# Kernel tuning notes

Hardware: AMD Instinct MI355X
Metric: run time of the kernel (lower is better)

## Reference

```python
import jax, jax.numpy as jnp
import numpy as np

N = 50000
E = 800000
IN_CH = 128
HID = 32
HEADS = 8
OUT_CH = 64
NEG_SLOPE = 0.2  # PyG GATConv default


def setup_inputs() -> dict:
    key = jax.random.key(0)
    ks = jax.random.split(key, 12)
    x = jax.random.normal(ks[0], (N, IN_CH), dtype=jnp.float32)
    edge_index = jax.random.randint(ks[1], (2, E), 0, N, dtype=jnp.int64)
    s = 0.1
    return {
        "x": x,
        "edge_index": edge_index,
        "W1": jax.random.normal(ks[2], (IN_CH, HEADS * HID), dtype=jnp.float32) * s,
        "att_src1": jax.random.normal(ks[3], (HEADS, HID), dtype=jnp.float32) * s,
        "att_dst1": jax.random.normal(ks[4], (HEADS, HID), dtype=jnp.float32) * s,
        "b1": jnp.zeros((HEADS * HID,), dtype=jnp.float32),
        "W2": jax.random.normal(ks[5], (HEADS * HID, OUT_CH), dtype=jnp.float32) * s,
        "att_src2": jax.random.normal(ks[6], (1, OUT_CH), dtype=jnp.float32) * s,
        "att_dst2": jax.random.normal(ks[7], (1, OUT_CH), dtype=jnp.float32) * s,
        "b2": jnp.zeros((OUT_CH,), dtype=jnp.float32),
    }


def _gat_layer(x, src, dst, n, W, a_src, a_dst, b, concat):
    # x: [N, F_in]; src/dst: [E']; W: [F_in, H*C]; a_*: [H, C]
    H, C = a_src.shape
    h = (x @ W).reshape(-1, H, C)                       # [N, H, C]
    alpha_s = jnp.einsum('nhc,hc->nh', h, a_src)        # [N, H]
    alpha_d = jnp.einsum('nhc,hc->nh', h, a_dst)        # [N, H]
    alpha = alpha_s[src] + alpha_d[dst]                 # [E', H]
    alpha = jax.nn.leaky_relu(alpha, NEG_SLOPE)
    # segment (per-destination-node) softmax over incoming edges
    m = jax.ops.segment_max(alpha, dst, num_segments=n)     # [n, H]
    e = jnp.exp(alpha - m[dst])
    denom = jax.ops.segment_sum(e, dst, num_segments=n)     # [n, H]
    coef = e / denom[dst]                                   # [E', H]
    msg = h[src] * coef[:, :, None]                         # [E', H, C]
    out = jax.ops.segment_sum(msg, dst, num_segments=n)     # [n, H, C]
    out = out.reshape(n, H * C) if concat else out.mean(axis=1)
    return out + b


def reference(x, edge_index, W1, att_src1, att_dst1, b1, W2, att_src2, att_dst2, b2):
    n = x.shape[0]
    # PyG GATConv default: add self-loops
    loop = jnp.arange(n, dtype=edge_index.dtype)
    src = jnp.concatenate([edge_index[0], loop])
    dst = jnp.concatenate([edge_index[1], loop])
    # eval mode: F.dropout and attention dropout are identity
    h = _gat_layer(x, src, dst, n, W1, att_src1, att_dst1, b1, concat=True)
    h = jax.nn.elu(h)
    out = _gat_layer(h, src, dst, n, W2, att_src2, att_dst2, b2, concat=False)
    return out
```

## Files before the change

### kernel.cpp

```cpp
#include <hip/hip_runtime.h>
#include <hip/hip_bf16.h>
#include <math.h>

#define N_NODES 50000
#define N_EDGES 800000
#define E_TOT   (N_EDGES + N_NODES)
#define IN_CH 128
#define HID 32
#define HEADS 8
#define OUT_CH 64
#define NEG_SLOPE 0.2f
#define NBLK 196
#define RBLK 3321
#define G1BLK 3125
#define G2BLK 782
#define ABLK 12500
#define LOG2E 1.4426950408889634f

typedef __attribute__((ext_vector_type(8))) short bf16x8;
typedef __attribute__((ext_vector_type(4))) float f32x4;

__device__ __forceinline__ float lrelu(float x) { return x > 0.f ? x : NEG_SLOPE * x; }
__device__ __forceinline__ float explrelu(float z) {
    return exp2f(fmaxf(z * LOG2E, z * (NEG_SLOPE * LOG2E)));
}

__device__ __forceinline__ unsigned short f2bf(float f) {
    unsigned int u = __float_as_uint(f);
    unsigned int r = (u + 0x7FFFu + ((u >> 16) & 1u)) >> 16;
    return (unsigned short)r;
}
__device__ __forceinline__ float bf2f(unsigned short u) {
    return __uint_as_float(((unsigned int)u) << 16);
}
__device__ __forceinline__ float bflo(unsigned int u) {
    return __uint_as_float(u << 16);
}
__device__ __forceinline__ float bfhi(unsigned int u) {
    return __uint_as_float(u & 0xFFFF0000u);
}

__global__ void w1cast_kernel(const float* __restrict__ W1,
                              unsigned short* __restrict__ W1t) {
    int i = blockIdx.x * 256 + threadIdx.x;
    int col = i >> 7, k = i & 127;
    W1t[i] = f2bf(W1[k * 256 + col]);
}

__device__ __forceinline__ void gemm1_body(
    int blk, int t,
    const float* __restrict__ x, const unsigned short* __restrict__ W1t,
    const float* __restrict__ att_s, const float* __restrict__ att_d,
    unsigned short* __restrict__ h1b, float* __restrict__ as1, float* __restrict__ ad1) {
    int lane = t & 63;
    int w = t >> 6;
    int lrow = lane & 15;
    int kg = lane >> 4;
    int row0 = blk * 16;
    int gr = row0 + lrow;
    f32x4 acc0 = {0.f, 0.f, 0.f, 0.f};
    f32x4 acc1 = {0.f, 0.f, 0.f, 0.f};
    f32x4 acc2 = {0.f, 0.f, 0.f, 0.f};
    f32x4 acc3 = {0.f, 0.f, 0.f, 0.f};
#pragma unroll
    for (int ks = 0; ks < 4; ++ks) {
        const float* ap = &x[(size_t)gr * IN_CH + ks * 32 + kg * 8];
        float4 a0 = *(const float4*)ap;
        float4 a1 = *(const float4*)(ap + 4);
        union { bf16x8 v; unsigned int u[4]; } A;
        A.u[0] = ((unsigned)f2bf(a0.y) << 16) | f2bf(a0.x);
        A.u[1] = ((unsigned)f2bf(a0.w) << 16) | f2bf(a0.z);
        A.u[2] = ((unsigned)f2bf(a1.y) << 16) | f2bf(a1.x);
        A.u[3] = ((unsigned)f2bf(a1.w) << 16) | f2bf(a1.z);
        union { bf16x8 v; uint4 u; } B0, B1, B2, B3;
        int kb = ks * 32 + kg * 8;
        B0.u = *(const uint4*)&W1t[(size_t)(w * 64 + 0 * 16 + lrow) * IN_CH + kb];
        B1.u = *(const uint4*)&W1t[(size_t)(w * 64 + 1 * 16 + lrow) * IN_CH + kb];
        B2.u = *(const uint4*)&W1t[(size_t)(w * 64 + 2 * 16 + lrow) * IN_CH + kb];
        B3.u = *(const uint4*)&W1t[(size_t)(w * 64 + 3 * 16 + lrow) * IN_CH + kb];
        acc0 = __builtin_amdgcn_mfma_f32_16x16x32_bf16(A.v, B0.v, acc0, 0, 0, 0);
        acc1 = __builtin_amdgcn_mfma_f32_16x16x32_bf16(A.v, B1.v, acc1, 0, 0, 0);
        acc2 = __builtin_amdgcn_mfma_f32_16x16x32_bf16(A.v, B2.v, acc2, 0, 0, 0);
        acc3 = __builtin_amdgcn_mfma_f32_16x16x32_bf16(A.v, B3.v, acc3, 0, 0, 0);
    }
    float s0 = att_s[w * 64 + 0 * 16 + lrow], d0 = att_d[w * 64 + 0 * 16 + lrow];
    float s1 = att_s[w * 64 + 1 * 16 + lrow], d1 = att_d[w * 64 + 1 * 16 + lrow];
    float s2 = att_s[w * 64 + 2 * 16 + lrow], d2 = att_d[w * 64 + 2 * 16 + lrow];
    float s3 = att_s[w * 64 + 3 * 16 + lrow], d3 = att_d[w * 64 + 3 * 16 + lrow];
#pragma unroll
    for (int r = 0; r < 4; ++r) {
        int orow = row0 + kg * 4 + r;
        h1b[(size_t)orow * 256 + w * 64 +  0 + lrow] = f2bf(acc0[r]);
        h1b[(size_t)orow * 256 + w * 64 + 16 + lrow] = f2bf(acc1[r]);
        h1b[(size_t)orow * 256 + w * 64 + 32 + lrow] = f2bf(acc2[r]);
        h1b[(size_t)orow * 256 + w * 64 + 48 + lrow] = f2bf(acc3[r]);
        float p0 = acc0[r] * s0 + acc1[r] * s1;
        float q0 = acc0[r] * d0 + acc1[r] * d1;
        float p1 = acc2[r] * s2 + acc3[r] * s3;
        float q1 = acc2[r] * d2 + acc3[r] * d3;
        p0 += __shfl_xor(p0, 1); q0 += __shfl_xor(q0, 1);
        p1 += __shfl_xor(p1, 1); q1 += __shfl_xor(q1, 1);
        p0 += __shfl_xor(p0, 2); q0 += __shfl_xor(q0, 2);
        p1 += __shfl_xor(p1, 2); q1 += __shfl_xor(q1, 2);
        p0 += __shfl_xor(p0, 4); q0 += __shfl_xor(q0, 4);
        p1 += __shfl_xor(p1, 4); q1 += __shfl_xor(q1, 4);
        p0 += __shfl_xor(p0, 8); q0 += __shfl_xor(q0, 8);
        p1 += __shfl_xor(p1, 8); q1 += __shfl_xor(q1, 8);
        if (lrow == 0) {
            as1[orow * HEADS + 2 * w]     = p0;
            ad1[orow * HEADS + 2 * w]     = q0;
            as1[orow * HEADS + 2 * w + 1] = p1;
            ad1[orow * HEADS + 2 * w + 1] = q1;
        }
    }
}

__global__ __launch_bounds__(256) void fused1_kernel(
    const int* __restrict__ ei, int* __restrict__ deg2, int* __restrict__ rank,
    const float* __restrict__ x, const unsigned short* __restrict__ W1t,
    const float* __restrict__ att_s, const float* __restrict__ att_d,
    unsigned short* __restrict__ h1b, float* __restrict__ as1, float* __restrict__ ad1,
    const float* __restrict__ W2, unsigned short* __restrict__ W2t) {
    int b = blockIdx.x;
    if (b < RBLK) {
        int e = b * 256 + threadIdx.x;
        if (e < E_TOT) {
            int d = (e < N_EDGES) ? ei[N_EDGES + e] : (e - N_EDGES);
            rank[e] = atomicAdd(&deg2[d * 16], 1);
        }
    } else if (b < RBLK + G1BLK) {
        gemm1_body(b - RBLK, threadIdx.x, x, W1t, att_s, att_d, h1b, as1, ad1);
    } else {
        int i = (b - RBLK - G1BLK) * 256 + threadIdx.x;
        int col = i >> 8, k = i & 255;
        W2t[i] = f2bf(W2[k * 64 + col]);
    }
}

__global__ void scan1_kernel(const int* __restrict__ deg2, int* __restrict__ off,
                             int* __restrict__ bsum) {
    __shared__ int s[256];
    int b = blockIdx.x, t = threadIdx.x, g = b * 256 + t;
    int v = (g < N_NODES) ? deg2[g * 16] : 0;
    s[t] = v;
    __syncthreads();
    for (int d = 1; d < 256; d <<= 1) {
        int o = (t >= d) ? s[t - d] : 0;
        __syncthreads();
        s[t] += o;
        __syncthreads();
    }
    if (g < N_NODES) off[g] = s[t] - v;
    if (t == 255) bsum[b] = s[t];
}

__global__ void scan2_kernel(int* __restrict__ bsum, int nb) {
    __shared__ int s[256];
    int t = threadIdx.x;
    int v = (t < nb) ? bsum[t] : 0;
    s[t] = v;
    __syncthreads();
    for (int d = 1; d < 256; d <<= 1) {
        int o = (t >= d) ? s[t - d] : 0;
        __syncthreads();
        s[t] += o;
        __syncthreads();
    }
    if (t < nb) bsum[t] = s[t] - v;
}

__global__ void scan3_kernel(int* __restrict__ off, const int* __restrict__ bsum) {
    int b = blockIdx.x, t = threadIdx.x, g = b * 256 + t;
    if (g < N_NODES) off[g] += bsum[b];
    if (g == 0) off[N_NODES] = E_TOT;
}

__global__ void place_kernel(const int* __restrict__ ei, const int* __restrict__ off,
                             const int* __restrict__ rank, int* __restrict__ ssrc) {
    int e = blockIdx.x * blockDim.x + threadIdx.x;
    if (e >= E_TOT) return;
    int s, d;
    if (e < N_EDGES) { s = ei[e]; d = ei[N_EDGES + e]; }
    else             { s = d = e - N_EDGES; }
    ssrc[off[d] + rank[e]] = s;
}

__global__ __launch_bounds__(256) void agg1_kernel(
    const int* __restrict__ off, const int* __restrict__ ssrc,
    const unsigned short* __restrict__ h1b, const float* __restrict__ as1,
    const float* __restrict__ ad1, const float* __restrict__ b1,
    unsigned short* __restrict__ houtb) {
    int t = threadIdx.x;
    int lane = t & 63;
    int n = blockIdx.x * 4 + (t >> 6);
    int h    = lane >> 3;
    int e8   = lane & 7;
    int c    = lane & 31;
    int hh   = c >> 2;
    int half = lane >> 5;
    int start = off[n], end = off[n + 1];
    int last = end - 1;
    float ad_w = ad1[n * HEADS + e8];
    float acc[8];
#pragma unroll
    for (int j = 0; j < 8; ++j) acc[j] = 0.f;
    float den = 0.f;
    int sv = ssrc[min(start + e8, last)];
    int se = __shfl(sv, h);
    float av = as1[se * HEADS + e8];
    const unsigned short* base = h1b + c * 8;
    uint4 g0 = *(const uint4*)&base[(unsigned)__shfl(sv, 0 + half) * 256];
    uint4 g1 = *(const uint4*)&base[(unsigned)__shfl(sv, 2 + half) * 256];
    uint4 g2 = *(const uint4*)&base[(unsigned)__shfl(sv, 4 + half) * 256];
    uint4 g3 = *(const uint4*)&base[(unsigned)__shfl(sv, 6 + half) * 256];
    for (int i = start; i < end; i += 8) {
        int inext = i + 8;
        int sv_n = ssrc[min(inext + e8, last)];
        int se_n = __shfl(sv_n, h);
        float av_n = as1[se_n * HEADS + e8];
        uint4 n0 = *(const uint4*)&base[(unsigned)__shfl(sv_n, 0 + half) * 256];
        uint4 n1 = *(const uint4*)&base[(unsigned)__shfl(sv_n, 2 + half) * 256];
        uint4 n2 = *(const uint4*)&base[(unsigned)__shfl(sv_n, 4 + half) * 256];
        uint4 n3 = *(const uint4*)&base[(unsigned)__shfl(sv_n, 6 + half) * 256];
        float wv = explrelu(av + ad_w);
        float w0 = __shfl(wv, (0 + half) * 8 + hh);
        float w1 = __shfl(wv, (2 + half) * 8 + hh);
        float w2 = __shfl(wv, (4 + half) * 8 + hh);
        float w3 = __shfl(wv, (6 + half) * 8 + hh);
        w0 = (i + 0 + half < end) ? w0 : 0.f;
        w1 = (i + 2 + half < end) ? w1 : 0.f;
        w2 = (i + 4 + half < end) ? w2 : 0.f;
        w3 = (i + 6 + half < end) ? w3 : 0.f;
        den += w0 + w1 + w2 + w3;
        acc[0] = fmaf(w0, bflo(g0.x), acc[0]); acc[1] = fmaf(w0, bfhi(g0.x), acc[1]);
        acc[2] = fmaf(w0, bflo(g0.y), acc[2]); acc[3] = fmaf(w0, bfhi(g0.y), acc[3]);
        acc[4] = fmaf(w0, bflo(g0.z), acc[4]); acc[5] = fmaf(w0, bfhi(g0.z), acc[5]);
        acc[6] = fmaf(w0, bflo(g0.w), acc[6]); acc[7] = fmaf(w0, bfhi(g0.w), acc[7]);
        acc[0] = fmaf(w1, bflo(g1.x), acc[0]); acc[1] = fmaf(w1, bfhi(g1.x), acc[1]);
        acc[2] = fmaf(w1, bflo(g1.y), acc[2]); acc[3] = fmaf(w1, bfhi(g1.y), acc[3]);
        acc[4] = fmaf(w1, bflo(g1.z), acc[4]); acc[5] = fmaf(w1, bfhi(g1.z), acc[5]);
        acc[6] = fmaf(w1, bflo(g1.w), acc[6]); acc[7] = fmaf(w1, bfhi(g1.w), acc[7]);
        acc[0] = fmaf(w2, bflo(g2.x), acc[0]); acc[1] = fmaf(w2, bfhi(g2.x), acc[1]);
        acc[2] = fmaf(w2, bflo(g2.y), acc[2]); acc[3] = fmaf(w2, bfhi(g2.y), acc[3]);
        acc[4] = fmaf(w2, bflo(g2.z), acc[4]); acc[5] = fmaf(w2, bfhi(g2.z), acc[5]);
        acc[6] = fmaf(w2, bflo(g2.w), acc[6]); acc[7] = fmaf(w2, bfhi(g2.w), acc[7]);
        acc[0] = fmaf(w3, bflo(g3.x), acc[0]); acc[1] = fmaf(w3, bfhi(g3.x), acc[1]);
        acc[2] = fmaf(w3, bflo(g3.y), acc[2]); acc[3] = fmaf(w3, bfhi(g3.y), acc[3]);
        acc[4] = fmaf(w3, bflo(g3.z), acc[4]); acc[5] = fmaf(w3, bfhi(g3.z), acc[5]);
        acc[6] = fmaf(w3, bflo(g3.w), acc[6]); acc[7] = fmaf(w3, bfhi(g3.w), acc[7]);
        g0 = n0; g1 = n1; g2 = n2; g3 = n3;
        sv = sv_n; av = av_n;
    }
#pragma unroll
    for (int j = 0; j < 8; ++j) acc[j] += __shfl_xor(acc[j], 32);
    den += __shfl_xor(den, 32);
    if (lane < 32) {
        float r = __builtin_amdgcn_rcpf(den);
        float4 b0 = *(const float4*)&b1[c * 8];
        float4 b4 = *(const float4*)&b1[c * 8 + 4];
        float v0 = fmaf(acc[0], r, b0.x);
        float v1 = fmaf(acc[1], r, b0.y);
        float v2 = fmaf(acc[2], r, b0.z);
        float v3 = fmaf(acc[3], r, b0.w);
        float v4 = fmaf(acc[4], r, b4.x);
        float v5 = fmaf(acc[5], r, b4.y);
        float v6 = fmaf(acc[6], r, b4.z);
        float v7 = fmaf(acc[7], r, b4.w);
        v0 = v0 > 0.f ? v0 : expm1f(v0);
        v1 = v1 > 0.f ? v1 : expm1f(v1);
        v2 = v2 > 0.f ? v2 : expm1f(v2);
        v3 = v3 > 0.f ? v3 : expm1f(v3);
        v4 = v4 > 0.f ? v4 : expm1f(v4);
        v5 = v5 > 0.f ? v5 : expm1f(v5);
        v6 = v6 > 0.f ? v6 : expm1f(v6);
        v7 = v7 > 0.f ? v7 : expm1f(v7);
        uint4 ob;
        ob.x = (unsigned)f2bf(v0) | ((unsigned)f2bf(v1) << 16);
        ob.y = (unsigned)f2bf(v2) | ((unsigned)f2bf(v3) << 16);
        ob.z = (unsigned)f2bf(v4) | ((unsigned)f2bf(v5) << 16);
        ob.w = (unsigned)f2bf(v6) | ((unsigned)f2bf(v7) << 16);
        *(uint4*)&houtb[(unsigned)n * 256 + c * 8] = ob;
    }
}

__global__ __launch_bounds__(256) void gemm2_mfma(
    const unsigned short* __restrict__ hinb, const unsigned short* __restrict__ W2t,
    const float* __restrict__ att_s2, const float* __restrict__ att_d2,
    unsigned short* __restrict__ h2b, float* __restrict__ as2, float* __restrict__ ad2) {
    int t = threadIdx.x;
    int lane = t & 63;
    int w = t >> 6;
    int lrow = lane & 15;
    int kg = lane >> 4;
    int row0 = blockIdx.x * 64 + w * 16;
    int gr = min(row0 + lrow, N_NODES - 1);
    f32x4 acc0 = {0.f, 0.f, 0.f, 0.f};
    f32x4 acc1 = {0.f, 0.f, 0.f, 0.f};
    f32x4 acc2 = {0.f, 0.f, 0.f, 0.f};
    f32x4 acc3 = {0.f, 0.f, 0.f, 0.f};
#pragma unroll
    for (int ks = 0; ks < 8; ++ks) {
        int kb = ks * 32 + kg * 8;
        union { bf16x8 v; uint4 u; } A, B0, B1, B2, B3;
        A.u  = *(const uint4*)&hinb[(size_t)gr * 256 + kb];
        B0.u = *(const uint4*)&W2t[(size_t)(0 * 16 + lrow) * 256 + kb];
        B1.u = *(const uint4*)&W2t[(size_t)(1 * 16 + lrow) * 256 + kb];
        B2.u = *(const uint4*)&W2t[(size_t)(2 * 16 + lrow) * 256 + kb];
        B3.u = *(const uint4*)&W2t[(size_t)(3 * 16 + lrow) * 256 + kb];
        acc0 = __builtin_amdgcn_mfma_f32_16x16x32_bf16(A.v, B0.v, acc0, 0, 0, 0);
        acc1 = __builtin_amdgcn_mfma_f32_16x16x32_bf16(A.v, B1.v, acc1, 0, 0, 0);
        acc2 = __builtin_amdgcn_mfma_f32_16x16x32_bf16(A.v, B2.v, acc2, 0, 0, 0);
        acc3 = __builtin_amdgcn_mfma_f32_16x16x32_bf16(A.v, B3.v, acc3, 0, 0, 0);
    }
    float s0 = att_s2[ 0 + lrow], d0 = att_d2[ 0 + lrow];
    float s1 = att_s2[16 + lrow], d1 = att_d2[16 + lrow];
    float s2 = att_s2[32 + lrow], d2 = att_d2[32 + lrow];
    float s3 = att_s2[48 + lrow], d3 = att_d2[48 + lrow];
#pragma unroll
    for (int r = 0; r < 4; ++r) {
        int orow = row0 + kg * 4 + r;
        float p = acc0[r] * s0 + acc1[r] * s1 + acc2[r] * s2 + acc3[r] * s3;
        float q = acc0[r] * d0 + acc1[r] * d1 + acc2[r] * d2 + acc3[r] * d3;
        p += __shfl_xor(p, 1); q += __shfl_xor(q, 1);
        p += __shfl_xor(p, 2); q += __shfl_xor(q, 2);
        p += __shfl_xor(p, 4); q += __shfl_xor(q, 4);
        p += __shfl_xor(p, 8); q += __shfl_xor(q, 8);
        if (orow < N_NODES) {
            h2b[(size_t)orow * 64 +  0 + lrow] = f2bf(acc0[r]);
            h2b[(size_t)orow * 64 + 16 + lrow] = f2bf(acc1[r]);
            h2b[(size_t)orow * 64 + 32 + lrow] = f2bf(acc2[r]);
            h2b[(size_t)orow * 64 + 48 + lrow] = f2bf(acc3[r]);
            if (lrow == 0) { as2[orow] = p; ad2[orow] = q; }
        }
    }
}

__global__ __launch_bounds__(256) void agg2_kernel(
    const int* __restrict__ off, const int* __restrict__ ssrc,
    const unsigned short* __restrict__ h2b, const float* __restrict__ as2,
    const float* __restrict__ ad2, const float* __restrict__ b2,
    float* __restrict__ out) {
    int t = threadIdx.x;
    int lane = t & 63;
    int e8 = lane & 7;
    int q = lane & 15;
    int quarter = lane >> 4;
    int n = blockIdx.x * 4 + (t >> 6);
    int start = off[n], end = off[n + 1];
    int last = end - 1;
    float adv = ad2[n];
    float acc[4];
#pragma unroll
    for (int j = 0; j < 4; ++j) acc[j] = 0.f;
    float den = 0.f;
    int sv = ssrc[min(start + e8, last)];
    float av = as2[sv];
    for (int i = start; i < end; i += 8) {
        int inext = i + 8;
        int sv_n = ssrc[min(inext + e8, last)];
        float av_n = as2[sv_n];
        float wv = explrelu(av + adv);
#pragma unroll
        for (int k = 0; k < 2; ++k) {
            int me = 4 * k + quarter;
            float wj = __shfl(wv, me);
            int   sj = __shfl(sv, me);
            wj = (i + me < end) ? wj : 0.f;
            uint2 u = *(const uint2*)&h2b[(unsigned)sj * 64 + q * 4];
            den += wj;
            acc[0] = fmaf(wj, bflo(u.x), acc[0]);
            acc[1] = fmaf(wj, bfhi(u.x), acc[1]);
            acc[2] = fmaf(wj, bflo(u.y), acc[2]);
            acc[3] = fmaf(wj, bfhi(u.y), acc[3]);
        }
        sv = sv_n; av = av_n;
    }
#pragma unroll
    for (int j = 0; j < 4; ++j) {
        acc[j] += __shfl_xor(acc[j], 16);
        acc[j] += __shfl_xor(acc[j], 32);
    }
    den += __shfl_xor(den, 16);
    den += __shfl_xor(den, 32);
    if (lane < 16) {
        float r = __builtin_amdgcn_rcpf(den);
        float4 bv = *(const float4*)&b2[q * 4];
        float4 o;
        o.x = fmaf(acc[0], r, bv.x);
        o.y = fmaf(acc[1], r, bv.y);
        o.z = fmaf(acc[2], r, bv.z);
        o.w = fmaf(acc[3], r, bv.w);
        *(float4*)&out[(unsigned)n * 64 + q * 4] = o;
    }
}

extern "C" void kernel_launch(void* const* d_in, const int* in_sizes, int n_in,
                              void* d_out, int out_size, void* d_ws, size_t ws_size,
                              hipStream_t stream) {
    const float* x    = (const float*)d_in[0];
    const int*   ei   = (const int*)d_in[1];
    const float* W1   = (const float*)d_in[2];
    const float* ats1 = (const float*)d_in[3];
    const float* atd1 = (const float*)d_in[4];
    const float* b1   = (const float*)d_in[5];
    const float* W2   = (const float*)d_in[6];
    const float* ats2 = (const float*)d_in[7];
    const float* atd2 = (const float*)d_in[8];
    const float* b2   = (const float*)d_in[9];
    float* out = (float*)d_out;

    char* ws = (char*)d_ws;
    size_t o = 0;
    auto alloc = [&](size_t bytes) { size_t r = o; o = (o + bytes + 255) & ~255UL; return r; };
    unsigned short* h1b   = (unsigned short*)(ws + alloc((size_t)N_NODES * 256 * 2));
    unsigned short* h2inb = (unsigned short*)(ws + alloc((size_t)N_NODES * 256 * 2));
    unsigned short* h2b   = (unsigned short*)(ws + alloc((size_t)N_NODES * 64 * 2));
    unsigned short* W1t   = (unsigned short*)(ws + alloc((size_t)256 * 128 * 2));
    unsigned short* W2t   = (unsigned short*)(ws + alloc((size_t)64 * 256 * 2));
    float* as1  = (float*)(ws + alloc((size_t)N_NODES * HEADS * 4));
    float* ad1  = (float*)(ws + alloc((size_t)N_NODES * HEADS * 4));
    float* as2  = (float*)(ws + alloc((size_t)N_NODES * 4));
    float* ad2  = (float*)(ws + alloc((size_t)N_NODES * 4));
    int*   deg2 = (int*)(ws + alloc((size_t)N_NODES * 16 * 4));
    int*   off  = (int*)(ws + alloc((size_t)(N_NODES + 1) * 4));
    int*   bsum = (int*)(ws + alloc(256 * 4));
    int*   rank = (int*)(ws + alloc((size_t)E_TOT * 4));
    int*   ssrc = (int*)(ws + alloc((size_t)E_TOT * 4));

    (void)hipMemsetAsync(deg2, 0, (size_t)N_NODES * 16 * 4, stream);
    int eblk = (E_TOT + 255) / 256;

    w1cast_kernel<<<128, 256, 0, stream>>>(W1, W1t);
    fused1_kernel<<<RBLK + G1BLK + 64, 256, 0, stream>>>(
        ei, deg2, rank, x, W1t, ats1, atd1, h1b, as1, ad1, W2, W2t);
    scan1_kernel<<<NBLK, 256, 0, stream>>>(deg2, off, bsum);
    scan2_kernel<<<1, 256, 0, stream>>>(bsum, NBLK);
    scan3_kernel<<<NBLK, 256, 0, stream>>>(off, bsum);
    place_kernel<<<eblk, 256, 0, stream>>>(ei, off, rank, ssrc);

    agg1_kernel<<<ABLK, 256, 0, stream>>>(off, ssrc, h1b, as1, ad1, b1, h2inb);

    gemm2_mfma<<<G2BLK, 256, 0, stream>>>(h2inb, W2t, ats2, atd2, h2b, as2, ad2);
    agg2_kernel<<<ABLK, 256, 0, stream>>>(off, ssrc, h2b, as2, ad2, b2, out);
}
```

Baseline: 219.0 us.

## Split degree counters into eight sub-histograms to reduce atomic contention

Replaces the single padded per-node degree counter (stride 16) with eight sub-counters per node, chosen by edge index mod 8, so concurrent atomics on hot destinations spread across separate addresses. The scan kernel now folds the eight sub-counts into per-node totals and turns each sub-counter into a local exclusive offset, which the placement kernel adds to the rank. The memset footprint halves, but scan1 reads and writes eight strided arrays and place does an extra gather per edge.

```diff
diff --git a/kernel.cpp b/kernel.cpp
--- a/kernel.cpp
+++ b/kernel.cpp
@@ -116,7 +116,7 @@
 }
 
 __global__ __launch_bounds__(256) void fused1_kernel(
-    const int* __restrict__ ei, int* __restrict__ deg2, int* __restrict__ rank,
+    const int* __restrict__ ei, int* __restrict__ deg8, int* __restrict__ rank,
     const float* __restrict__ x, const unsigned short* __restrict__ W1t,
     const float* __restrict__ att_s, const float* __restrict__ att_d,
     unsigned short* __restrict__ h1b, float* __restrict__ as1, float* __restrict__ ad1,
@@ -126,7 +126,8 @@
         int e = b * 256 + threadIdx.x;
         if (e < E_TOT) {
             int d = (e < N_EDGES) ? ei[N_EDGES + e] : (e - N_EDGES);
-            rank[e] = atomicAdd(&deg2[d * 16], 1);
+            int r = e & 7;
+            rank[e] = atomicAdd(&deg8[r * N_NODES + d], 1);
         }
     } else if (b < RBLK + G1BLK) {
         gemm1_body(b - RBLK, threadIdx.x, x, W1t, att_s, att_d, h1b, as1, ad1);
@@ -137,11 +138,21 @@
     }
 }
 
-__global__ void scan1_kernel(const int* __restrict__ deg2, int* __restrict__ off,
+__global__ void scan1_kernel(int* __restrict__ deg8, int* __restrict__ off,
                              int* __restrict__ bsum) {
     __shared__ int s[256];
     int b = blockIdx.x, t = threadIdx.x, g = b * 256 + t;
-    int v = (g < N_NODES) ? deg2[g * 16] : 0;
+    int v = 0;
+    if (g < N_NODES) {
+        int run = 0;
+#pragma unroll
+        for (int r = 0; r < 8; ++r) {
+            int c = deg8[r * N_NODES + g];
+            deg8[r * N_NODES + g] = run;
+            run += c;
+        }
+        v = run;
+    }
     s[t] = v;
     __syncthreads();
     for (int d = 1; d < 256; d <<= 1) {
@@ -176,13 +187,15 @@
 }
 
 __global__ void place_kernel(const int* __restrict__ ei, const int* __restrict__ off,
-                             const int* __restrict__ rank, int* __restrict__ ssrc) {
+                             const int* __restrict__ deg8, const int* __restrict__ rank,
+                             int* __restrict__ ssrc) {
     int e = blockIdx.x * blockDim.x + threadIdx.x;
     if (e >= E_TOT) return;
     int s, d;
     if (e < N_EDGES) { s = ei[e]; d = ei[N_EDGES + e]; }
     else             { s = d = e - N_EDGES; }
-    ssrc[off[d] + rank[e]] = s;
+    int r = e & 7;
+    ssrc[off[d] + deg8[r * N_NODES + d] + rank[e]] = s;
 }
 
 __global__ __launch_bounds__(256) void agg1_kernel(
@@ -421,22 +434,22 @@
     float* ad1  = (float*)(ws + alloc((size_t)N_NODES * HEADS * 4));
     float* as2  = (float*)(ws + alloc((size_t)N_NODES * 4));
     float* ad2  = (float*)(ws + alloc((size_t)N_NODES * 4));
-    int*   deg2 = (int*)(ws + alloc((size_t)N_NODES * 16 * 4));
+    int*   deg8 = (int*)(ws + alloc((size_t)N_NODES * 8 * 4));
     int*   off  = (int*)(ws + alloc((size_t)(N_NODES + 1) * 4));
     int*   bsum = (int*)(ws + alloc(256 * 4));
     int*   rank = (int*)(ws + alloc((size_t)E_TOT * 4));
     int*   ssrc = (int*)(ws + alloc((size_t)E_TOT * 4));
 
-    (void)hipMemsetAsync(deg2, 0, (size_t)N_NODES * 16 * 4, stream);
+    (void)hipMemsetAsync(deg8, 0, (size_t)N_NODES * 8 * 4, stream);
     int eblk = (E_TOT + 255) / 256;
 
     w1cast_kernel<<<128, 256, 0, stream>>>(W1, W1t);
     fused1_kernel<<<RBLK + G1BLK + 64, 256, 0, stream>>>(
-        ei, deg2, rank, x, W1t, ats1, atd1, h1b, as1, ad1, W2, W2t);
-    scan1_kernel<<<NBLK, 256, 0, stream>>>(deg2, off, bsum);
+        ei, deg8, rank, x, W1t, ats1, atd1, h1b, as1, ad1, W2, W2t);
+    scan1_kernel<<<NBLK, 256, 0, stream>>>(deg8, off, bsum);
     scan2_kernel<<<1, 256, 0, stream>>>(bsum, NBLK);
     scan3_kernel<<<NBLK, 256, 0, stream>>>(off, bsum);
-    place_kernel<<<eblk, 256, 0, stream>>>(ei, off, rank, ssrc);
+    place_kernel<<<eblk, 256, 0, stream>>>(ei, off, deg8, rank, ssrc);
 
     agg1_kernel<<<ABLK, 256, 0, stream>>>(off, ssrc, h1b, as1, ad1, b1, h2inb);
 
```

Result: no change. 222.4 us (+1.5%).
